# Performance work log

Hardware: AMD Instinct MI355X
Metric: run time of the kernel (lower is better)

## Reference

```python
import jax, jax.numpy as jnp
import numpy as np

B, S, D, H = 2, 2048, 1024, 16
DK = D // H


def setup_inputs() -> dict:
    key = jax.random.key(0)
    ks = jax.random.split(key, 12)
    s = 1.0 / np.sqrt(D)
    inp = {
        "query": jax.random.normal(ks[0], (B, S, D), jnp.float32),
        "key_": jax.random.normal(ks[1], (B, S, D), jnp.float32),
        "value": jax.random.normal(ks[2], (B, S, D), jnp.float32),
        # causal mask, broadcast over heads: [B, 1, S, S]
        "mask": jnp.broadcast_to(jnp.tril(jnp.ones((S, S), bool)), (B, 1, S, S)),
        "W_q": jax.random.uniform(ks[3], (D, D), jnp.float32, -s, s),
        "b_q": jax.random.uniform(ks[4], (D,), jnp.float32, -s, s),
        "W_k": jax.random.uniform(ks[5], (D, D), jnp.float32, -s, s),
        "b_k": jax.random.uniform(ks[6], (D,), jnp.float32, -s, s),
        "W_v": jax.random.uniform(ks[7], (D, D), jnp.float32, -s, s),
        "b_v": jax.random.uniform(ks[8], (D,), jnp.float32, -s, s),
        "W_o": jax.random.uniform(ks[9], (D, D), jnp.float32, -s, s),
        "b_o": jax.random.uniform(ks[10], (D,), jnp.float32, -s, s),
    }
    return inp


def reference(query, key_, value, mask, W_q, b_q, W_k, b_k, W_v, b_v, W_o, b_o):
    b = query.shape[0]
    # linear projections (torch Linear: x @ W.T + b)
    Q = query @ W_q.T + b_q
    K = key_ @ W_k.T + b_k
    V = value @ W_v.T + b_v
    # [b, S, H, dk] -> [b, H, S, dk]
    Q = Q.reshape(b, -1, H, DK).transpose(0, 2, 1, 3)
    K = K.reshape(b, -1, H, DK).transpose(0, 2, 1, 3)
    V = V.reshape(b, -1, H, DK).transpose(0, 2, 1, 3)
    scores = jnp.einsum("bhqd,bhkd->bhqk", Q, K) / jnp.sqrt(jnp.float32(DK))
    scores = jnp.where(mask, scores, -jnp.inf)
    attn = jax.nn.softmax(scores, axis=-1)
    out = jnp.einsum("bhqk,bhkd->bhqd", attn, V)
    out = out.transpose(0, 2, 1, 3).reshape(b, -1, D)
    return out @ W_o.T + b_o
```

## Files before the change

kernel.cpp:

```cpp
#include <hip/hip_runtime.h>
#include <hip/hip_bf16.h>
#include <stdint.h>

#define B_ 2
#define S_ 2048
#define D_ 1024
#define H_ 16
#define DK_ 64

typedef __attribute__((ext_vector_type(4))) float floatx4;
typedef __attribute__((ext_vector_type(8))) short shortx8;
typedef __attribute__((ext_vector_type(4))) short shortx4;
typedef unsigned short ushort_t;

__device__ inline ushort_t f2bf(float f) {
  union { float f; unsigned u; } v; v.f = f;
  unsigned r = v.u + 0x7FFFu + ((v.u >> 16) & 1u);
  return (ushort_t)(r >> 16);
}

__device__ inline unsigned pack2bf(float lo, float hi) {
  return __builtin_amdgcn_perm(__float_as_uint(hi), __float_as_uint(lo), 0x07060302u);
}

__device__ inline shortx4 mk_sx4(unsigned lo, unsigned hi) {
  union { unsigned u[2]; shortx4 s; } v; v.u[0] = lo; v.u[1] = hi; return v.s;
}

__device__ inline shortx8 cat44(shortx4 a, shortx4 b) {
  union { shortx4 s4[2]; shortx8 s8; } v; v.s4[0] = a; v.s4[1] = b; return v.s8;
}

__device__ inline float fast_exp2(float x) {
#if __has_builtin(__builtin_amdgcn_exp2f)
  return __builtin_amdgcn_exp2f(x);
#else
  return __expf(0.69314718056f * x);
#endif
}

__device__ inline void gload_lds16(const void* g, void* l) {
  __builtin_amdgcn_global_load_lds(
      (const __attribute__((address_space(1))) unsigned int*)g,
      (__attribute__((address_space(3))) unsigned int*)l, 16, 0, 0);
}

struct ConvArgs {
  const float* src[7];
  ushort_t* dst[7];
};

__global__ __launch_bounds__(256) void convert_kernel(ConvArgs a) {
  int blk = blockIdx.x;
  int seg, bis;
  if (blk < 3072) { seg = blk >> 10; bis = blk & 1023; }
  else { int bb = blk - 3072; seg = 3 + (bb >> 8); bis = bb & 255; }
  const float4* src = (const float4*)(a.src[seg]) + (size_t)bis * 1024;
  ushort4* dst = (ushort4*)(a.dst[seg]) + (size_t)bis * 1024;
#pragma unroll
  for (int i = 0; i < 4; ++i) {
    int idx = i * 256 + threadIdx.x;
    float4 v = src[idx];
    ushort4 o;
    o.x = f2bf(v.x); o.y = f2bf(v.y); o.z = f2bf(v.z); o.w = f2bf(v.w);
    dst[idx] = o;
  }
}

template <int TM>
__device__ inline void gemm_bk64_core(const ushort_t* __restrict__ A,
                                      const ushort_t* __restrict__ W,
                                      const float* __restrict__ bias,
                                      float scl,
                                      void* __restrict__ outp,
                                      int m0, int n0, int N, int K, int outmode) {
  constexpr int GA = TM / 8;
  constexpr int GB = 16;
  constexpr int GW = (GA + GB) / 4;
  constexpr int MI = TM / 32;
  constexpr int BUFB = (TM + 128) * 128;
  __shared__ uint4 smem4[2 * BUFB / 16];
  char* smem = (char*)&smem4[0];

  const int tid = threadIdx.x;
  const int wave = tid >> 6;
  const int lane = tid & 63;
  const int quad = lane >> 4;
  const int l16 = lane & 15;
  const int wm = (wave >> 1) * (TM / 2);
  const int wn = (wave & 1) * 64;

  floatx4 acc[MI][4] = {};

  const ushort_t* gsrc[GW];
  int ldst[GW];
#pragma unroll
  for (int i = 0; i < GW; ++i) {
    int g = wave * GW + i;
    int r8 = lane >> 3;
    int cs = ((lane & 7) ^ r8) * 8;
    if (g < GA) {
      gsrc[i] = A + (size_t)(m0 + g * 8 + r8) * K + cs;
      ldst[i] = g * 1024 + lane * 16;
    } else {
      gsrc[i] = W + (size_t)(n0 + (g - GA) * 8 + r8) * K + cs;
      ldst[i] = TM * 128 + (g - GA) * 1024 + lane * 16;
    }
  }

#pragma unroll
  for (int i = 0; i < GW; ++i) gload_lds16(gsrc[i], smem + ldst[i]);

  const int niter = K >> 6;
  for (int j = 0; j < niter; ++j) {
    __syncthreads();
    if (j + 1 < niter) {
      const int ko = (j + 1) * 64;
      char* bufn = smem + ((j + 1) & 1) * BUFB;
#pragma unroll
      for (int i = 0; i < GW; ++i) gload_lds16(gsrc[i] + ko, bufn + ldst[i]);
    }
    const char* aT = smem + (j & 1) * BUFB;
    const char* bT = aT + TM * 128;
    shortx8 af[MI][2], bf[4][2];
#pragma unroll
    for (int ks = 0; ks < 2; ++ks) {
      const int co = ((ks * 4 + quad) ^ (l16 & 7)) * 16;
#pragma unroll
      for (int mi = 0; mi < MI; ++mi)
        af[mi][ks] = *(const shortx8*)(aT + (wm + mi * 16 + l16) * 128 + co);
#pragma unroll
      for (int ni = 0; ni < 4; ++ni)
        bf[ni][ks] = *(const shortx8*)(bT + (wn + ni * 16 + l16) * 128 + co);
    }
#pragma unroll
    for (int ks = 0; ks < 2; ++ks)
#pragma unroll
      for (int mi = 0; mi < MI; ++mi)
#pragma unroll
        for (int ni = 0; ni < 4; ++ni)
          acc[mi][ni] = __builtin_amdgcn_mfma_f32_16x16x32_bf16(af[mi][ks], bf[ni][ks], acc[mi][ni], 0, 0, 0);
  }

#pragma unroll
  for (int ni = 0; ni < 4; ++ni) {
    int n = n0 + wn + ni * 16 + l16;
    float bv = bias[n];
#pragma unroll
    for (int mi = 0; mi < MI; ++mi) {
      if (outmode == 2) {
        int m = m0 + wm + mi * 16 + quad * 4;
        int b = m >> 11;
        int s = (m & 2047 & ~31) | (quad * 8 + mi * 4);
        ushort_t* dst = (ushort_t*)outp + (((size_t)(b * 1024 + n)) << 11) + s;
        uint2 pk;
        pk.x = (unsigned)f2bf(acc[mi][ni][0] + bv) |
               ((unsigned)f2bf(acc[mi][ni][1] + bv) << 16);
        pk.y = (unsigned)f2bf(acc[mi][ni][2] + bv) |
               ((unsigned)f2bf(acc[mi][ni][3] + bv) << 16);
        *(uint2*)(dst) = pk;
      } else {
#pragma unroll
        for (int r = 0; r < 4; ++r) {
          int m = m0 + wm + mi * 16 + quad * 4 + r;
          float v = (acc[mi][ni][r] + bv) * scl;
          if (outmode == 1) ((float*)outp)[(size_t)m * N + n] = v;
          else ((ushort_t*)outp)[(size_t)m * N + n] = f2bf(v);
        }
      }
    }
  }
}

struct QkvArgs {
  const ushort_t* A[3];
  const ushort_t* W[3];
  const float* bias[3];
  ushort_t* out[3];
  float scale[3];
};

__global__ __launch_bounds__(256) void gemm_qkv_kernel(QkvArgs a) {
  int z = blockIdx.z;
  int m0 = (blockIdx.x * 8 + (blockIdx.y >> 3)) * 64;
  int n0 = (blockIdx.y & 7) * 128;
  gemm_bk64_core<64>(a.A[z], a.W[z], a.bias[z], a.scale[z], a.out[z],
                     m0, n0, D_, D_, z == 2 ? 2 : 0);
}

__global__ __launch_bounds__(256) void gemm_out_kernel(const ushort_t* __restrict__ A,
                                                       const ushort_t* __restrict__ W,
                                                       const float* __restrict__ bias,
                                                       float* __restrict__ out) {
  int m0 = (blockIdx.x * 8 + (blockIdx.y >> 3)) * 64;
  int n0 = (blockIdx.y & 7) * 128;
  gemm_bk64_core<64>(A, W, bias, 1.0f, out, m0, n0, D_, D_, 1);
}

__global__ __launch_bounds__(256, 4) void attn_kernel(const ushort_t* __restrict__ Qp,
                                                      const ushort_t* __restrict__ Kp,
                                                      const ushort_t* __restrict__ Vt,
                                                      ushort_t* __restrict__ O) {
  const int id = blockIdx.x;
  const int h = id & 15;
  const int u = (id >> 4) & 31;
  const int b = id >> 9;
  const int qt = b ? u : 31 - u;
  const int q0 = qt * 64;
  const int tid = threadIdx.x;
  const int wave = tid >> 6;
  const int lane = tid & 63;
  const int quad = lane >> 4;
  const int l16 = lane & 15;

  __shared__ ushort_t smem[2][8192];

  const size_t hoff = (size_t)h * DK_;

  shortx8 qf[2];
  {
    const ushort_t* qrow = Qp + ((size_t)b * S_ + q0 + wave * 16 + l16) * D_ + hoff;
    qf[0] = *(const shortx8*)(qrow + quad * 8);
    qf[1] = *(const shortx8*)(qrow + 32 + quad * 8);
  }

  const int r8 = lane >> 3;
  const int cs8 = ((lane & 7) ^ r8) * 8;
  const ushort_t* kb[2];
  const ushort_t* vb[2];
  int kdst[2], vdst[2];
#pragma unroll
  for (int g = 0; g < 2; ++g) {
    const int tr = wave * 16 + g * 8 + r8;
    kb[g] = Kp + ((size_t)b * S_ + tr) * D_ + hoff + cs8;
    vb[g] = Vt + ((size_t)(b * H_ + h) * 64 + tr) * (size_t)S_ + cs8;
    kdst[g] = (wave * 16 + g * 8) * 64 + lane * 8;
    vdst[g] = 4096 + (wave * 16 + g * 8) * 64 + lane * 8;
  }

  floatx4 oacc[4] = {};
  float l_run = 0.f;
  const int nj = qt + 1;

#pragma unroll
  for (int g = 0; g < 2; ++g) {
    gload_lds16(kb[g], &smem[0][kdst[g]]);
    gload_lds16(vb[g], &smem[0][vdst[g]]);
  }

  for (int j = 0; j < nj; ++j) {
    __syncthreads();
    if (j + 1 < nj) {
      ushort_t* bufn = smem[(j + 1) & 1];
      const size_t ko = (size_t)(j + 1) * 64 * D_;
      const int vo = (j + 1) * 64;
#pragma unroll
      for (int g = 0; g < 2; ++g) {
        gload_lds16(kb[g] + ko, bufn + kdst[g]);
        gload_lds16(vb[g] + vo, bufn + vdst[g]);
      }
    }
    const ushort_t* k_lds = smem[j & 1];
    const ushort_t* v_lds = smem[j & 1] + 4096;

    floatx4 sacc[4];
    __builtin_amdgcn_s_setprio(1);
#pragma unroll
    for (int kkb = 0; kkb < 4; ++kkb) {
      const ushort_t* krow = k_lds + (kkb * 16 + l16) * 64;
      shortx8 af0 = *(const shortx8*)(krow + (quad ^ (l16 & 7)) * 8);
      shortx8 af1 = *(const shortx8*)(krow + ((4 | quad) ^ (l16 & 7)) * 8);
      floatx4 acc = {0.f, 0.f, 0.f, 0.f};
      acc = __builtin_amdgcn_mfma_f32_16x16x32_bf16(af0, qf[0], acc, 0, 0, 0);
      acc = __builtin_amdgcn_mfma_f32_16x16x32_bf16(af1, qf[1], acc, 0, 0, 0);
      sacc[kkb] = acc;
    }
    __builtin_amdgcn_s_setprio(0);

    const int kbase = j * 64;
    if (kbase + 63 > q0 + wave * 16) {
      const int qg = q0 + wave * 16 + l16;
#pragma unroll
      for (int kkb = 0; kkb < 4; ++kkb)
#pragma unroll
        for (int r = 0; r < 4; ++r)
          if (kbase + kkb * 16 + quad * 4 + r > qg) sacc[kkb][r] = -3.0e38f;
    }

    shortx4 pf[4];
    {
      float psum = 0.f;
#pragma unroll
      for (int kkb = 0; kkb < 4; ++kkb) {
        float p0 = fast_exp2(sacc[kkb][0]);
        float p1 = fast_exp2(sacc[kkb][1]);
        float p2 = fast_exp2(sacc[kkb][2]);
        float p3 = fast_exp2(sacc[kkb][3]);
        psum += (p0 + p1) + (p2 + p3);
        pf[kkb] = mk_sx4(pack2bf(p0, p1), pack2bf(p2, p3));
      }
      l_run += psum;
    }

    __builtin_amdgcn_s_setprio(1);
#pragma unroll
    for (int kp = 0; kp < 2; ++kp) {
      const shortx8 pf8 = cat44(pf[kp * 2], pf[kp * 2 + 1]);
      const int jj = ((kp * 4 + quad) ^ (l16 & 7)) * 8;
#pragma unroll
      for (int db = 0; db < 4; ++db) {
        const shortx8 vf8 = *(const shortx8*)(v_lds + (db * 16 + l16) * 64 + jj);
        oacc[db] = __builtin_amdgcn_mfma_f32_16x16x32_bf16(vf8, pf8, oacc[db], 0, 0, 0);
      }
    }
    __builtin_amdgcn_s_setprio(0);
  }

  __syncthreads();
  ushort_t* sm = &smem[0][0];
  {
    float l0 = l_run;
    l0 += __shfl_xor(l0, 16);
    l0 += __shfl_xor(l0, 32);
    float inv_l = 1.0f / l0;
    int row = wave * 16 + l16;
#pragma unroll
    for (int db = 0; db < 4; ++db) {
#pragma unroll
      for (int rr = 0; rr < 2; ++rr) {
        unsigned pk = pack2bf(oacc[db][rr * 2] * inv_l, oacc[db][rr * 2 + 1] * inv_l);
        *(unsigned*)(sm + row * 72 + db * 16 + quad * 4 + rr * 2) = pk;
      }
    }
  }
  __syncthreads();
  {
    int r = tid >> 2, c = (tid & 3) * 16;
    const ushort_t* src = sm + r * 72 + c;
    ushort_t* dst = O + ((size_t)b * S_ + q0 + r) * D_ + hoff + c;
    uint4 v0 = *(const uint4*)(src);
    uint4 v1 = *(const uint4*)(src + 8);
    *(uint4*)(dst) = v0;
    *(uint4*)(dst + 8) = v1;
  }
}

extern "C" void kernel_launch(void* const* d_in, const int* in_sizes, int n_in,
                              void* d_out, int out_size, void* d_ws, size_t ws_size,
                              hipStream_t stream) {
  (void)in_sizes; (void)n_in; (void)out_size; (void)ws_size;
  char* ws = (char*)d_ws;
  ushort_t* xq = (ushort_t*)(ws + 0);
  ushort_t* xk = (ushort_t*)(ws + 8388608);
  ushort_t* xv = (ushort_t*)(ws + 16777216);
  ushort_t* wq = (ushort_t*)(ws + 25165824);
  ushort_t* wk = (ushort_t*)(ws + 27262976);
  ushort_t* wv = (ushort_t*)(ws + 29360128);
  ushort_t* wo = (ushort_t*)(ws + 31457280);
  ushort_t* Qp = (ushort_t*)(ws + 33554432);
  ushort_t* Kp = (ushort_t*)(ws + 41943040);
  ushort_t* Vt = (ushort_t*)(ws + 50331648);
  ushort_t* O = xq;

  ConvArgs ca;
  ca.src[0] = (const float*)d_in[0];  ca.dst[0] = xq;
  ca.src[1] = (const float*)d_in[1];  ca.dst[1] = xk;
  ca.src[2] = (const float*)d_in[2];  ca.dst[2] = xv;
  ca.src[3] = (const float*)d_in[4];  ca.dst[3] = wq;
  ca.src[4] = (const float*)d_in[6];  ca.dst[4] = wk;
  ca.src[5] = (const float*)d_in[8];  ca.dst[5] = wv;
  ca.src[6] = (const float*)d_in[10]; ca.dst[6] = wo;
  convert_kernel<<<dim3(4096), dim3(256), 0, stream>>>(ca);

  QkvArgs qa;
  qa.A[0] = xq; qa.W[0] = wq; qa.bias[0] = (const float*)d_in[5]; qa.out[0] = Qp;
  qa.A[1] = xk; qa.W[1] = wk; qa.bias[1] = (const float*)d_in[7]; qa.out[1] = Kp;
  qa.A[2] = xv; qa.W[2] = wv; qa.bias[2] = (const float*)d_in[9]; qa.out[2] = Vt;
  qa.scale[0] = 0.125f * 1.44269504089f;
  qa.scale[1] = 1.0f;
  qa.scale[2] = 1.0f;
  gemm_qkv_kernel<<<dim3(8, 64, 3), dim3(256), 0, stream>>>(qa);

  attn_kernel<<<dim3(1024), dim3(256), 0, stream>>>(Qp, Kp, Vt, O);

  gemm_out_kernel<<<dim3(8, 64, 1), dim3(256), 0, stream>>>(
      O, wo, (const float*)d_in[11], (float*)d_out);
}
```

Measured before the change: 217.4 us.

## Double attention query tile to 128 rows per block for K/V reuse

Each attention block now handles 128 query rows, with each wave covering two 16-row groups, so every K/V tile loaded into LDS feeds twice as many MFMAs. The grid is halved and launch bounds drop to 2 blocks per SM to leave room for the extra accumulator registers. Waves skip KV tiles that lie entirely above their causal diagonal. The risks are lower occupancy, fewer blocks to fill the device, and more causal load imbalance, since waves within a block now sit idle on different numbers of tiles.

```diff
diff --git a/kernel.cpp b/kernel.cpp
--- a/kernel.cpp
+++ b/kernel.cpp
@@ -197,16 +197,16 @@
   gemm_bk64_core<64>(A, W, bias, 1.0f, out, m0, n0, D_, D_, 1);
 }
 
-__global__ __launch_bounds__(256, 4) void attn_kernel(const ushort_t* __restrict__ Qp,
+__global__ __launch_bounds__(256, 2) void attn_kernel(const ushort_t* __restrict__ Qp,
                                                       const ushort_t* __restrict__ Kp,
                                                       const ushort_t* __restrict__ Vt,
                                                       ushort_t* __restrict__ O) {
   const int id = blockIdx.x;
   const int h = id & 15;
-  const int u = (id >> 4) & 31;
-  const int b = id >> 9;
-  const int qt = b ? u : 31 - u;
-  const int q0 = qt * 64;
+  const int u = (id >> 4) & 15;
+  const int b = id >> 8;
+  const int qt = b ? u : 15 - u;
+  const int q0 = qt * 128;
   const int tid = threadIdx.x;
   const int wave = tid >> 6;
   const int lane = tid & 63;
@@ -217,11 +217,12 @@
 
   const size_t hoff = (size_t)h * DK_;
 
-  shortx8 qf[2];
-  {
-    const ushort_t* qrow = Qp + ((size_t)b * S_ + q0 + wave * 16 + l16) * D_ + hoff;
-    qf[0] = *(const shortx8*)(qrow + quad * 8);
-    qf[1] = *(const shortx8*)(qrow + 32 + quad * 8);
+  shortx8 qf[2][2];
+#pragma unroll
+  for (int grp = 0; grp < 2; ++grp) {
+    const ushort_t* qrow = Qp + ((size_t)b * S_ + q0 + wave * 32 + grp * 16 + l16) * D_ + hoff;
+    qf[grp][0] = *(const shortx8*)(qrow + quad * 8);
+    qf[grp][1] = *(const shortx8*)(qrow + 32 + quad * 8);
   }
 
   const int r8 = lane >> 3;
@@ -238,9 +239,10 @@
     vdst[g] = 4096 + (wave * 16 + g * 8) * 64 + lane * 8;
   }
 
-  floatx4 oacc[4] = {};
-  float l_run = 0.f;
-  const int nj = qt + 1;
+  floatx4 oacc[2][4] = {};
+  float l_run[2] = {0.f, 0.f};
+  const int nj = 2 * (qt + 1);
+  const int qwave_max = q0 + wave * 32 + 31;
 
 #pragma unroll
   for (int g = 0; g < 2; ++g) {
@@ -260,57 +262,67 @@
         gload_lds16(vb[g] + vo, bufn + vdst[g]);
       }
     }
+    const int kbase = j * 64;
+    if (kbase > qwave_max) continue;
     const ushort_t* k_lds = smem[j & 1];
     const ushort_t* v_lds = smem[j & 1] + 4096;
 
-    floatx4 sacc[4];
+    floatx4 sacc[2][4];
     __builtin_amdgcn_s_setprio(1);
 #pragma unroll
     for (int kkb = 0; kkb < 4; ++kkb) {
       const ushort_t* krow = k_lds + (kkb * 16 + l16) * 64;
       shortx8 af0 = *(const shortx8*)(krow + (quad ^ (l16 & 7)) * 8);
       shortx8 af1 = *(const shortx8*)(krow + ((4 | quad) ^ (l16 & 7)) * 8);
-      floatx4 acc = {0.f, 0.f, 0.f, 0.f};
-      acc = __builtin_amdgcn_mfma_f32_16x16x32_bf16(af0, qf[0], acc, 0, 0, 0);
-      acc = __builtin_amdgcn_mfma_f32_16x16x32_bf16(af1, qf[1], acc, 0, 0, 0);
-      sacc[kkb] = acc;
+#pragma unroll
+      for (int grp = 0; grp < 2; ++grp) {
+        floatx4 acc = {0.f, 0.f, 0.f, 0.f};
+        acc = __builtin_amdgcn_mfma_f32_16x16x32_bf16(af0, qf[grp][0], acc, 0, 0, 0);
+        acc = __builtin_amdgcn_mfma_f32_16x16x32_bf16(af1, qf[grp][1], acc, 0, 0, 0);
+        sacc[grp][kkb] = acc;
+      }
     }
     __builtin_amdgcn_s_setprio(0);
 
-    const int kbase = j * 64;
-    if (kbase + 63 > q0 + wave * 16) {
-      const int qg = q0 + wave * 16 + l16;
-#pragma unroll
-      for (int kkb = 0; kkb < 4; ++kkb)
-#pragma unroll
-        for (int r = 0; r < 4; ++r)
-          if (kbase + kkb * 16 + quad * 4 + r > qg) sacc[kkb][r] = -3.0e38f;
-    }
-
-    shortx4 pf[4];
-    {
+#pragma unroll
+    for (int grp = 0; grp < 2; ++grp) {
+      if (kbase + 63 > q0 + wave * 32 + grp * 16) {
+        const int qg = q0 + wave * 32 + grp * 16 + l16;
+#pragma unroll
+        for (int kkb = 0; kkb < 4; ++kkb)
+#pragma unroll
+          for (int r = 0; r < 4; ++r)
+            if (kbase + kkb * 16 + quad * 4 + r > qg) sacc[grp][kkb][r] = -3.0e38f;
+      }
+    }
+
+    shortx4 pf[2][4];
+#pragma unroll
+    for (int grp = 0; grp < 2; ++grp) {
       float psum = 0.f;
 #pragma unroll
       for (int kkb = 0; kkb < 4; ++kkb) {
-        float p0 = fast_exp2(sacc[kkb][0]);
-        float p1 = fast_exp2(sacc[kkb][1]);
-        float p2 = fast_exp2(sacc[kkb][2]);
-        float p3 = fast_exp2(sacc[kkb][3]);
+        float p0 = fast_exp2(sacc[grp][kkb][0]);
+        float p1 = fast_exp2(sacc[grp][kkb][1]);
+        float p2 = fast_exp2(sacc[grp][kkb][2]);
+        float p3 = fast_exp2(sacc[grp][kkb][3]);
         psum += (p0 + p1) + (p2 + p3);
-        pf[kkb] = mk_sx4(pack2bf(p0, p1), pack2bf(p2, p3));
-      }
-      l_run += psum;
+        pf[grp][kkb] = mk_sx4(pack2bf(p0, p1), pack2bf(p2, p3));
+      }
+      l_run[grp] += psum;
     }
 
     __builtin_amdgcn_s_setprio(1);
 #pragma unroll
     for (int kp = 0; kp < 2; ++kp) {
-      const shortx8 pf8 = cat44(pf[kp * 2], pf[kp * 2 + 1]);
+      const shortx8 pf8a = cat44(pf[0][kp * 2], pf[0][kp * 2 + 1]);
+      const shortx8 pf8b = cat44(pf[1][kp * 2], pf[1][kp * 2 + 1]);
       const int jj = ((kp * 4 + quad) ^ (l16 & 7)) * 8;
 #pragma unroll
       for (int db = 0; db < 4; ++db) {
         const shortx8 vf8 = *(const shortx8*)(v_lds + (db * 16 + l16) * 64 + jj);
-        oacc[db] = __builtin_amdgcn_mfma_f32_16x16x32_bf16(vf8, pf8, oacc[db], 0, 0, 0);
+        oacc[0][db] = __builtin_amdgcn_mfma_f32_16x16x32_bf16(vf8, pf8a, oacc[0][db], 0, 0, 0);
+        oacc[1][db] = __builtin_amdgcn_mfma_f32_16x16x32_bf16(vf8, pf8b, oacc[1][db], 0, 0, 0);
       }
     }
     __builtin_amdgcn_s_setprio(0);
@@ -318,30 +330,35 @@
 
   __syncthreads();
   ushort_t* sm = &smem[0][0];
-  {
-    float l0 = l_run;
+#pragma unroll
+  for (int grp = 0; grp < 2; ++grp) {
+    float l0 = l_run[grp];
     l0 += __shfl_xor(l0, 16);
     l0 += __shfl_xor(l0, 32);
     float inv_l = 1.0f / l0;
-    int row = wave * 16 + l16;
+    int row = wave * 32 + grp * 16 + l16;
 #pragma unroll
     for (int db = 0; db < 4; ++db) {
 #pragma unroll
       for (int rr = 0; rr < 2; ++rr) {
-        unsigned pk = pack2bf(oacc[db][rr * 2] * inv_l, oacc[db][rr * 2 + 1] * inv_l);
+        unsigned pk = pack2bf(oacc[grp][db][rr * 2] * inv_l, oacc[grp][db][rr * 2 + 1] * inv_l);
         *(unsigned*)(sm + row * 72 + db * 16 + quad * 4 + rr * 2) = pk;
       }
     }
   }
   __syncthreads();
   {
-    int r = tid >> 2, c = (tid & 3) * 16;
+    int r = tid >> 1, c = (tid & 1) * 32;
     const ushort_t* src = sm + r * 72 + c;
     ushort_t* dst = O + ((size_t)b * S_ + q0 + r) * D_ + hoff + c;
     uint4 v0 = *(const uint4*)(src);
     uint4 v1 = *(const uint4*)(src + 8);
+    uint4 v2 = *(const uint4*)(src + 16);
+    uint4 v3 = *(const uint4*)(src + 24);
     *(uint4*)(dst) = v0;
     *(uint4*)(dst + 8) = v1;
+    *(uint4*)(dst + 16) = v2;
+    *(uint4*)(dst + 24) = v3;
   }
 }
 
@@ -381,7 +398,7 @@
   qa.scale[2] = 1.0f;
   gemm_qkv_kernel<<<dim3(8, 64, 3), dim3(256), 0, stream>>>(qa);
 
-  attn_kernel<<<dim3(1024), dim3(256), 0, stream>>>(Qp, Kp, Vt, O);
+  attn_kernel<<<dim3(512), dim3(256), 0, stream>>>(Qp, Kp, Vt, O);
 
   gemm_out_kernel<<<dim3(8, 64, 1), dim3(256), 0, stream>>>(
       O, wo, (const float*)d_in[11], (float*)d_out);
```

Result: no change. 218.6 us (+0.6%).
